# Kernel tuning notes

Measured on AMD Instinct MI355X. Metric: run time of the kernel, lower is better.

Reference implementation:

```python
import jax, jax.numpy as jnp
import numpy as np

B, G, K, N, M, E, L = 8, 512, 64, 1024, 128, 4, 5

def _lin(x, w, b):
    return x @ w.T + b

def setup_inputs():
    key = jax.random.key(0)
    ks = jax.random.split(key, 20)
    def nrm(k, shape, s=1.0):
        return jax.random.normal(k, shape, dtype=jnp.float32) * s
    def lin_p(k, out_d, in_d):
        k1, k2 = jax.random.split(k)
        s = 1.0 / float(np.sqrt(in_d))
        return nrm(k1, (out_d, in_d), s), nrm(k2, (out_d,), s)
    inp = {}
    inp["z"] = nrm(ks[0], (B, G, K, M), 0.5)
    inp["hs_grid"] = nrm(ks[1], (B, G, M))
    inp["hs_key"] = nrm(ks[2], (B, K, M))
    inp["lig_rep"] = nrm(ks[3], (B, E))
    inp["hs_rec"] = nrm(ks[4], (B, N, M))
    inp["w_Rl"] = jnp.ones((1,), dtype=jnp.float32)
    inp["w_mask"] = jax.random.randint(ks[5], (B, K), 0, 2)
    dims = {"wra": (M, M), "wrh": (M, M), "wla": (M, M), "wlh": (M, M),
            "z1": (1, M), "wcR": (M, M), "wcl": (M, M), "kR": (M, M),
            "mapL": (L, 2 * M + E), "fin": (1, L)}
    for i, nm in enumerate(dims):
        w, b = lin_p(ks[6 + i], *dims[nm])
        inp[nm + "_w"] = w
        inp[nm + "_b"] = b
    return inp

def reference(z, hs_grid, hs_key, lig_rep, hs_rec, w_Rl, w_mask,
              wra_w, wra_b, wrh_w, wrh_b, wla_w, wla_b, wlh_w, wlh_b,
              z1_w, z1_b, wcR_w, wcR_b, wcl_w, wcl_b, kR_w, kR_b,
              mapL_w, mapL_b, fin_w, fin_b):
    exp_z = jnp.exp(z)                                    # [B,G,K,M]
    zr = exp_z / exp_z.sum(axis=-2, keepdims=True)        # pseudo-softmax over K
    ra = jnp.einsum('bgkm,bkm->bgm', zr, hs_key)          # [B,G,M]
    zl = exp_z / exp_z.sum(axis=-3, keepdims=True)        # pseudo-softmax over G
    la = jnp.einsum('bgkm,bgm->bkm', zl, hs_grid)         # [B,K,M]
    ra_rh = _lin(ra, wra_w, wra_b) + _lin(hs_grid, wrh_w, wrh_b)  # [B,G,M]
    la_lh = _lin(la, wla_w, wla_b) + _lin(hs_key, wlh_w, wlh_b)   # [B,K,M]
    att = _lin(z, z1_w, z1_b)[..., 0]                     # [B,G,K]
    att_l = jax.nn.softmax(att, axis=2).sum(axis=1)       # [B,K]
    att_r = jax.nn.softmax(att, axis=1).sum(axis=2)       # [B,G]
    key_rep = jnp.einsum('bk,bkm->bm', att_l, la_lh)      # [B,M]
    grid_rep = jnp.einsum('bg,bgm->bm', att_r, ra_rh)     # [B,M]
    Rh = _lin(hs_rec, wcR_w, wcR_b)                       # [B,N,M]
    lh = _lin(hs_key, wcl_w, wcl_b)                       # [B,K,M]
    z_Rl = jnp.einsum('bnh,bkh->bnk', Rh, lh)             # [B,N,K]
    masked = jnp.where(w_mask[:, None, :] == 0, jnp.float32(-1e10), w_Rl * z_Rl)
    z_Rl = jax.nn.softmax(masked, axis=1)                 # softmax over N
    kfr = jnp.einsum('bnk,bnh->bkh', z_Rl, hs_rec)        # [B,K,M]
    kfr = _lin(kfr, kR_w, kR_b)
    kfr = jnp.einsum('bk,bkh->bh', att_l, kfr)            # [B,M]
    key_rep = key_rep + kfr
    pair_rep = jnp.concatenate([key_rep, lig_rep, grid_rep], axis=1)  # [B,2M+E]
    pair_rep = _lin(pair_rep, mapL_w, mapL_b)             # [B,L]
    return _lin(pair_rep, fin_w, fin_b)[..., 0]           # [B]
```

## Files before the change

### kernel.cpp

```cpp
#include <hip/hip_runtime.h>

#define Bb 8
#define Gg 512
#define Kk 64
#define Nn 1024
#define Mm 128
#define KM (Kk * Mm)
#define GPB 16
#define NCH (Gg / GPB)

struct P7 { const float* p[7]; };

__global__ __launch_bounds__(1024) void kA(
    const float* __restrict__ z, const float* __restrict__ hs_grid,
    const float* __restrict__ hs_key, const float* __restrict__ z1w,
    P7 ptrs, float* __restrict__ wT,
    float* __restrict__ raOut, float* __restrict__ attOut,
    float* __restrict__ laNum, float* __restrict__ laDen)
{
  __shared__ __align__(16) float smem[18432];
  const int bid = blockIdx.x;
  const int t = threadIdx.x;

  if (bid >= Bb * NCH) {
    float* tile = smem;
    const int r = bid - Bb * NCH;
    const int mat = r >> 4, tl = r & 15;
    const int xo = (tl & 3) * 32, y0 = (tl >> 2) * 32;
    const int tx = t & 31, ty = t >> 5;
    const float* src = ptrs.p[mat];
    float* dst = wT + (size_t)mat * Mm * Mm;
    tile[ty * 33 + tx] = src[(size_t)(y0 + ty) * Mm + xo + tx];
    __syncthreads();
    dst[(size_t)(xo + ty) * Mm + y0 + tx] = tile[tx * 33 + ty];
    return;
  }

  float* s_hskey  = smem;
  float* s_hsgrid = smem + 8192;
  float* s_rn     = smem + 10240;
  float* s_rd     = smem + 14336;

  const int b = bid >> 5;
  const int gblk = bid & 31;
  const int lane_m = t & 31;
  const int m4 = lane_m << 2;
  const int kgrp = t >> 5;
  const int wv = t >> 6;

  const float* hkb = hs_key + (size_t)b * KM;
  for (int idx = t; idx < KM; idx += 1024) s_hskey[idx] = hkb[idx];
  const float* hgb = hs_grid + ((size_t)b * Gg + gblk * GPB) * Mm;
  for (int idx = t; idx < GPB * Mm; idx += 1024) s_hsgrid[idx] = hgb[idx];

  const float zw0 = z1w[m4], zw1 = z1w[m4 + 1], zw2 = z1w[m4 + 2], zw3 = z1w[m4 + 3];

  float la_n[2][4], la_d[2][4];
#pragma unroll
  for (int i = 0; i < 2; ++i)
#pragma unroll
    for (int j = 0; j < 4; ++j) { la_n[i][j] = 0.f; la_d[i][j] = 0.f; }

  const float* zb = z + ((size_t)b * Gg + gblk * GPB) * (size_t)Mm * Kk;
  const int ofs0 = (kgrp * 2) * Mm + m4;
  const int ofs1 = ofs0 + Mm;
  float4 c0 = *reinterpret_cast<const float4*>(zb + ofs0);
  float4 c1 = *reinterpret_cast<const float4*>(zb + ofs1);

  __syncthreads();

  for (int gl = 0; gl < GPB; ++gl) {
    float4 n0 = c0, n1 = c1;
    if (gl < GPB - 1) {
      n0 = *reinterpret_cast<const float4*>(zb + (size_t)(gl + 1) * KM + ofs0);
      n1 = *reinterpret_cast<const float4*>(zb + (size_t)(gl + 1) * KM + ofs1);
    }
    const int g = gblk * GPB + gl;
    const float4 hg = *reinterpret_cast<const float4*>(s_hsgrid + gl * Mm + m4);
    float rn0 = 0, rn1 = 0, rn2 = 0, rn3 = 0, rd0 = 0, rd1 = 0, rd2 = 0, rd3 = 0;
#pragma unroll
    for (int i = 0; i < 2; ++i) {
      const float4 v = (i == 0) ? c0 : c1;
      const int k = kgrp * 2 + i;
      const float e0 = __expf(v.x), e1 = __expf(v.y), e2 = __expf(v.z), e3 = __expf(v.w);
      la_n[i][0] += e0 * hg.x; la_n[i][1] += e1 * hg.y; la_n[i][2] += e2 * hg.z; la_n[i][3] += e3 * hg.w;
      la_d[i][0] += e0;        la_d[i][1] += e1;        la_d[i][2] += e2;        la_d[i][3] += e3;
      const float4 hk = *reinterpret_cast<const float4*>(s_hskey + k * Mm + m4);
      rn0 += e0 * hk.x; rn1 += e1 * hk.y; rn2 += e2 * hk.z; rn3 += e3 * hk.w;
      rd0 += e0; rd1 += e1; rd2 += e2; rd3 += e3;
      float ap = v.x * zw0 + v.y * zw1 + v.z * zw2 + v.w * zw3;
      ap += __shfl_xor(ap, 16); ap += __shfl_xor(ap, 8); ap += __shfl_xor(ap, 4);
      ap += __shfl_xor(ap, 2);  ap += __shfl_xor(ap, 1);
      if (lane_m == 0) attOut[((size_t)b * Gg + g) * Kk + k] = ap;
    }
    rn0 += __shfl_xor(rn0, 32); rn1 += __shfl_xor(rn1, 32); rn2 += __shfl_xor(rn2, 32); rn3 += __shfl_xor(rn3, 32);
    rd0 += __shfl_xor(rd0, 32); rd1 += __shfl_xor(rd1, 32); rd2 += __shfl_xor(rd2, 32); rd3 += __shfl_xor(rd3, 32);
    float* rnB = s_rn + (gl & 1) * 2048;
    float* rdB = s_rd + (gl & 1) * 2048;
    if ((t & 63) < 32) {
      *reinterpret_cast<float4*>(rnB + wv * Mm + m4) = make_float4(rn0, rn1, rn2, rn3);
      *reinterpret_cast<float4*>(rdB + wv * Mm + m4) = make_float4(rd0, rd1, rd2, rd3);
    }
    __syncthreads();
    if (t < Mm) {
      float num = 0.f, den = 0.f;
#pragma unroll
      for (int ww = 0; ww < 16; ++ww) { num += rnB[ww * Mm + t]; den += rdB[ww * Mm + t]; }
      raOut[((size_t)b * Gg + g) * Mm + t] = num / den;
    }
    c0 = n0; c1 = n1;
  }

  const size_t base = ((size_t)(b * NCH + gblk)) * KM;
#pragma unroll
  for (int i = 0; i < 2; ++i) {
    const int k = kgrp * 2 + i;
    *reinterpret_cast<float4*>(laNum + base + k * Mm + m4) =
        make_float4(la_n[i][0], la_n[i][1], la_n[i][2], la_n[i][3]);
    *reinterpret_cast<float4*>(laDen + base + k * Mm + m4) =
        make_float4(la_d[i][0], la_d[i][1], la_d[i][2], la_d[i][3]);
  }
}

__global__ __launch_bounds__(256) void kB(
    const float* __restrict__ laNum, const float* __restrict__ laDen, float* __restrict__ la,
    const float* __restrict__ att, float* __restrict__ attlP,
    float* __restrict__ attrPM, float* __restrict__ attrPS,
    const float* __restrict__ hs_key, const float* __restrict__ wT,
    const float* __restrict__ wcR_w, const float* __restrict__ wcl_b,
    float* __restrict__ Lk)
{
  __shared__ __align__(16) float smem[1088];
  const int bid = blockIdx.x;
  const int t = threadIdx.x;

  if (bid < 256) {
    const int idx = bid * 256 + t;
    const int b = idx >> 13, r = idx & 8191;
    const float* np = laNum + (size_t)b * NCH * KM + r;
    const float* dp = laDen + (size_t)b * NCH * KM + r;
    float num = 0.f, den = 0.f;
#pragma unroll 8
    for (int p = 0; p < NCH; ++p) { num += np[(size_t)p * KM]; den += dp[(size_t)p * KM]; }
    la[idx] = num / den;
  } else if (bid < 320) {
    const int blk = bid - 256;
    const int b = blk >> 3, p = blk & 7;
    const int w = t >> 6, lane = t & 63;
    float acc = 0.f;
    for (int j = 0; j < 16; ++j) {
      const int g = p * 64 + w * 16 + j;
      const float a = att[((size_t)b * Gg + g) * Kk + lane];
      float mx = a;
      for (int off = 32; off; off >>= 1) mx = fmaxf(mx, __shfl_xor(mx, off));
      const float e = __expf(a - mx);
      float s = e;
      for (int off = 32; off; off >>= 1) s += __shfl_xor(s, off);
      acc += e / s;
    }
    float* sred = smem;
    sred[w * 64 + lane] = acc;
    __syncthreads();
    if (t < 64) attlP[(b * 8 + p) * 64 + t] = sred[t] + sred[64 + t] + sred[128 + t] + sred[192 + t];
  } else if (bid < 384) {
    const int blk = bid - 320;
    const int b = blk >> 3, gc = blk & 7;
    const int k = t & 63, j4 = t >> 6;
    float m = -1e30f, s = 0.f;
    for (int j = 0; j < 16; ++j) {
      const int g = gc * 64 + j4 * 16 + j;
      const float a = att[((size_t)b * Gg + g) * Kk + k];
      if (a > m) { s = s * __expf(m - a) + 1.0f; m = a; }
      else s += __expf(a - m);
    }
    float* sm = smem;
    float* ss = smem + 256;
    sm[j4 * 64 + k] = m; ss[j4 * 64 + k] = s;
    __syncthreads();
    if (t < 64) {
      float M = sm[t];
      for (int q = 1; q < 4; ++q) M = fmaxf(M, sm[q * 64 + t]);
      float S = 0.f;
      for (int q = 0; q < 4; ++q) S += ss[q * 64 + t] * __expf(sm[q * 64 + t] - M);
      attrPM[(b * 8 + gc) * 64 + t] = M;
      attrPS[(b * 8 + gc) * 64 + t] = S;
    }
  } else {
    const int blk = bid - 384;
    const int b = blk >> 3, k8 = blk & 7;
    float* s_lh = smem;
    const int m = t & 127;
    const int half = __builtin_amdgcn_readfirstlane(t >> 7);
    const float* wclT = wT + 5 * 16384;
    {
      const float* keyb = hs_key + ((size_t)b * Kk + k8 * 8 + half * 4) * Mm;
      float a0 = 0.f, a1 = 0.f, a2 = 0.f, a3 = 0.f;
      for (int h = 0; h < 128; ++h) {
        const float w = wclT[(size_t)h * Mm + m];
        const float r0v = keyb[h];
        const float r1v = keyb[128 + h];
        const float r2v = keyb[256 + h];
        const float r3v = keyb[384 + h];
        a0 += r0v * w; a1 += r1v * w; a2 += r2v * w; a3 += r3v * w;
      }
      const float bm = wcl_b[m];
      s_lh[(half * 4 + 0) * 132 + m] = a0 + bm;
      s_lh[(half * 4 + 1) * 132 + m] = a1 + bm;
      s_lh[(half * 4 + 2) * 132 + m] = a2 + bm;
      s_lh[(half * 4 + 3) * 132 + m] = a3 + bm;
    }
    __syncthreads();
    {
      const int h = m;
      const int r0 = half * 4;
      float b0 = 0.f, b1 = 0.f, b2 = 0.f, b3 = 0.f;
      for (int mq = 0; mq < 32; ++mq) {
        const float4 L0 = *reinterpret_cast<const float4*>(&s_lh[(r0 + 0) * 132 + mq * 4]);
        const float4 L1 = *reinterpret_cast<const float4*>(&s_lh[(r0 + 1) * 132 + mq * 4]);
        const float4 L2 = *reinterpret_cast<const float4*>(&s_lh[(r0 + 2) * 132 + mq * 4]);
        const float4 L3 = *reinterpret_cast<const float4*>(&s_lh[(r0 + 3) * 132 + mq * 4]);
        const float w0 = wcR_w[(size_t)(mq * 4 + 0) * Mm + h];
        const float w1 = wcR_w[(size_t)(mq * 4 + 1) * Mm + h];
        const float w2 = wcR_w[(size_t)(mq * 4 + 2) * Mm + h];
        const float w3 = wcR_w[(size_t)(mq * 4 + 3) * Mm + h];
        b0 += L0.x * w0 + L0.y * w1 + L0.z * w2 + L0.w * w3;
        b1 += L1.x * w0 + L1.y * w1 + L1.z * w2 + L1.w * w3;
        b2 += L2.x * w0 + L2.y * w1 + L2.z * w2 + L2.w * w3;
        b3 += L3.x * w0 + L3.y * w1 + L3.z * w2 + L3.w * w3;
      }
      const size_t ob = ((size_t)b * Kk + k8 * 8 + r0) * Mm + h;
      Lk[ob] = b0; Lk[ob + Mm] = b1; Lk[ob + 2 * Mm] = b2; Lk[ob + 3 * Mm] = b3;
    }
  }
}

__global__ __launch_bounds__(256) void kC(
    const float* __restrict__ att, const float* __restrict__ attrPM, const float* __restrict__ attrPS,
    float* __restrict__ att_r,
    const float* __restrict__ hs_rec, const float* __restrict__ Lk,
    const int* __restrict__ mask, const float* __restrict__ wRl,
    float* __restrict__ scores, float* __restrict__ pmT, float* __restrict__ psT)
{
  __shared__ __align__(16) float smem[4608];
  const int bid = blockIdx.x;
  const int t = threadIdx.x;

  if (bid < 64) {
    const int b = bid >> 3, gc = bid & 7;
    const int k = t & 63, grp = t >> 6;
    float* Mx = smem;
    float* S = smem + 64;
    if (t < 64) {
      float M = -1e30f;
      for (int p = 0; p < 8; ++p) M = fmaxf(M, attrPM[(b * 8 + p) * 64 + t]);
      float s = 0.f;
      for (int p = 0; p < 8; ++p) s += attrPS[(b * 8 + p) * 64 + t] * __expf(attrPM[(b * 8 + p) * 64 + t] - M);
      Mx[t] = M; S[t] = s;
    }
    __syncthreads();
    const float Mk = Mx[k], Sk = S[k];
    for (int j = 0; j < 16; ++j) {
      const int g = gc * 64 + grp * 16 + j;
      float p = __expf(att[((size_t)b * Gg + g) * Kk + k] - Mk) / Sk;
      for (int off = 32; off; off >>= 1) p += __shfl_xor(p, off);
      if (k == 0) att_r[b * Gg + g] = p;
    }
  } else {
    const int vb = bid - 64;
    const int b = vb >> 6, ntile = vb & 63;
    const int n0 = ntile * 16;
    const int k = t & 63;
    const int hq = __builtin_amdgcn_readfirstlane(t >> 6);
    float rLk[32];
    {
      const float* Lp = Lk + ((size_t)b * Kk + k) * Mm + hq * 32;
#pragma unroll
      for (int j = 0; j < 8; ++j) {
        const float4 v = *reinterpret_cast<const float4*>(Lp + j * 4);
        rLk[j * 4 + 0] = v.x; rLk[j * 4 + 1] = v.y;
        rLk[j * 4 + 2] = v.z; rLk[j * 4 + 3] = v.w;
      }
    }
    float acc[16];
    const float* rb = hs_rec + ((size_t)b * Nn + n0) * Mm + hq * 32;
#pragma unroll
    for (int r = 0; r < 16; ++r) {
      const float* rp = rb + r * Mm;
      float s = 0.f;
#pragma unroll
      for (int j = 0; j < 32; ++j) s += rp[j] * rLk[j];
      acc[r] = s;
    }
    float* s_acc = smem;
    float* s_m   = smem + 4096;
    float* s_s   = smem + 4352;
#pragma unroll
    for (int r = 0; r < 16; ++r) s_acc[(hq * 16 + r) * 64 + k] = acc[r];
    __syncthreads();
    const float wv = wRl[0];
    const bool msk = (mask[b * Kk + k] == 0);
    float m = -3.0e38f, ssum = 0.f;
    for (int q = 0; q < 4; ++q) {
      const int idx = q * 256 + t;
      const int r = idx >> 6, kk = idx & 63;
      float v = s_acc[r * 64 + kk] + s_acc[(16 + r) * 64 + kk] +
                s_acc[(32 + r) * 64 + kk] + s_acc[(48 + r) * 64 + kk];
      v = msk ? -1e10f : wv * v;
      scores[((size_t)b * Nn + n0 + r) * Kk + kk] = v;
      if (v > m) { ssum = ssum * __expf(m - v) + 1.0f; m = v; }
      else ssum += __expf(v - m);
    }
    s_m[hq * 64 + k] = m; s_s[hq * 64 + k] = ssum;
    __syncthreads();
    if (t < 64) {
      float M = fmaxf(fmaxf(s_m[t], s_m[64 + t]), fmaxf(s_m[128 + t], s_m[192 + t]));
      float S = 0.f;
#pragma unroll
      for (int q = 0; q < 4; ++q) S += s_s[q * 64 + t] * __expf(s_m[q * 64 + t] - M);
      pmT[((size_t)b * 64 + ntile) * 64 + t] = M;
      psT[((size_t)b * 64 + ntile) * 64 + t] = S;
    }
  }
}

__global__ __launch_bounds__(512) void kD(
    const float* __restrict__ scores, const float* __restrict__ hs_rec,
    const float* __restrict__ pmT, const float* __restrict__ psT,
    const float* __restrict__ attlP, const float* __restrict__ att_r,
    const float* __restrict__ ra, const float* __restrict__ hs_grid,
    const float* __restrict__ la, const float* __restrict__ hs_key,
    float* __restrict__ uP, float* __restrict__ w1P, float* __restrict__ w2P,
    float* __restrict__ w0P, float* __restrict__ v1, float* __restrict__ v2,
    float* __restrict__ sAv)
{
  __shared__ float sm[1280];
  __shared__ float s_attl[64];
  __shared__ float sM[64], sSi[64];
  const int bid = blockIdx.x;
  const int t = threadIdx.x;

  if (bid < 64) {
    const int b = bid >> 3, nc = bid & 7;
    if (t < 64) {
      float a = 0.f;
      for (int p = 0; p < 8; ++p) a += attlP[(b * 8 + p) * 64 + t];
      s_attl[t] = a;
      float M = -3.0e38f;
      for (int nt = 0; nt < 64; ++nt) M = fmaxf(M, pmT[((size_t)b * 64 + nt) * 64 + t]);
      float S = 0.f;
      for (int nt = 0; nt < 64; ++nt)
        S += psT[((size_t)b * 64 + nt) * 64 + t] * __expf(pmT[((size_t)b * 64 + nt) * 64 + t] - M);
      sM[t] = M; sSi[t] = 1.0f / S;
    }
    __syncthreads();
    const int n = t >> 2, ks = t & 3;
    const float* sc = scores + ((size_t)b * Nn + nc * 128 + n) * Kk + ks * 16;
    float qp = 0.f;
#pragma unroll
    for (int j = 0; j < 16; ++j) {
      const int k = ks * 16 + j;
      qp += s_attl[k] * __expf(sc[j] - sM[k]) * sSi[k];
    }
    sm[n * 4 + ks] = qp;
    __syncthreads();
    float* q = sm + 512;
    if (t < 128) q[t] = sm[t * 4] + sm[t * 4 + 1] + sm[t * 4 + 2] + sm[t * 4 + 3];
    __syncthreads();
    const int h = t & 127, nq = t >> 7;
    float acc = 0.f;
    const float* hr = hs_rec + ((size_t)b * Nn + nc * 128 + nq * 32) * Mm + h;
    for (int j = 0; j < 32; ++j) acc += q[nq * 32 + j] * hr[(size_t)j * Mm];
    float* red = sm + 640;
    red[nq * 128 + h] = acc;
    __syncthreads();
    if (t < 128) uP[((size_t)b * 8 + nc) * 128 + t] = red[t] + red[128 + t] + red[256 + t] + red[384 + t];
  } else if (bid < 128) {
    const int blk = bid - 64;
    const int b = blk >> 3, gc = blk & 7;
    float* s_ar = sm + 1152;
    if (t < 64) s_ar[t] = att_r[b * Gg + gc * 64 + t];
    __syncthreads();
    const int h = t & 127, gq = t >> 7;
    float a1 = 0.f, a2 = 0.f;
    const float* rp = ra + ((size_t)b * Gg + gc * 64 + gq * 16) * Mm + h;
    const float* gp = hs_grid + ((size_t)b * Gg + gc * 64 + gq * 16) * Mm + h;
    for (int j = 0; j < 16; ++j) {
      const float w = s_ar[gq * 16 + j];
      a1 += w * rp[(size_t)j * Mm];
      a2 += w * gp[(size_t)j * Mm];
    }
    float* r1 = sm;
    float* r2 = sm + 512;
    r1[gq * 128 + h] = a1; r2[gq * 128 + h] = a2;
    __syncthreads();
    if (t < 128) {
      w1P[((size_t)b * 8 + gc) * 128 + t] = r1[t] + r1[128 + t] + r1[256 + t] + r1[384 + t];
      w2P[((size_t)b * 8 + gc) * 128 + t] = r2[t] + r2[128 + t] + r2[256 + t] + r2[384 + t];
    }
    if (t == 0) {
      float s = 0.f;
      for (int j = 0; j < 64; ++j) s += s_ar[j];
      w0P[b * 8 + gc] = s;
    }
  } else {
    const int b = bid - 128;
    if (t < 64) {
      float a = 0.f;
      for (int p = 0; p < 8; ++p) a += attlP[(b * 8 + p) * 64 + t];
      s_attl[t] = a;
    }
    __syncthreads();
    const int h = t & 127, kq = t >> 7;
    float a1 = 0.f, a2 = 0.f;
    const float* lp = la + ((size_t)b * Kk + kq * 16) * Mm + h;
    const float* kp = hs_key + ((size_t)b * Kk + kq * 16) * Mm + h;
    for (int j = 0; j < 16; ++j) {
      const float w = s_attl[kq * 16 + j];
      a1 += w * lp[(size_t)j * Mm];
      a2 += w * kp[(size_t)j * Mm];
    }
    float* r1 = sm;
    float* r2 = sm + 512;
    r1[kq * 128 + h] = a1; r2[kq * 128 + h] = a2;
    __syncthreads();
    if (t < 128) {
      v1[b * 128 + t] = r1[t] + r1[128 + t] + r1[256 + t] + r1[384 + t];
      v2[b * 128 + t] = r2[t] + r2[128 + t] + r2[256 + t] + r2[384 + t];
    }
    if (t == 0) {
      float s = 0.f;
      for (int j = 0; j < 64; ++j) s += s_attl[j];
      sAv[b] = s;
    }
  }
}

__global__ __launch_bounds__(256) void kE(
    const float* __restrict__ uP, const float* __restrict__ w1P, const float* __restrict__ w2P,
    const float* __restrict__ w0P, const float* __restrict__ v1, const float* __restrict__ v2,
    const float* __restrict__ sAv, const float* __restrict__ wT,
    const float* __restrict__ wra_b, const float* __restrict__ wrh_b,
    const float* __restrict__ wla_b, const float* __restrict__ wlh_b,
    const float* __restrict__ kR_b, const float* __restrict__ lig_rep,
    const float* __restrict__ mapL_w, const float* __restrict__ mapL_b,
    const float* __restrict__ fin_w, const float* __restrict__ fin_b,
    float* __restrict__ out)
{
  __shared__ float sV1[128], sV2[128], sU[128], sW1[128], sW2[128];
  __shared__ float sPair[260];
  __shared__ float sRed[2][2][128];
  __shared__ float s5[8];
  __shared__ float sSc[2];
  const int b = blockIdx.x, t = threadIdx.x;
  const int m = t & 127, hf = t >> 7;

  if (t < 128) {
    float u = 0.f, w1 = 0.f, w2 = 0.f;
    for (int c = 0; c < 8; ++c) {
      u  += uP[((size_t)b * 8 + c) * 128 + t];
      w1 += w1P[((size_t)b * 8 + c) * 128 + t];
      w2 += w2P[((size_t)b * 8 + c) * 128 + t];
    }
    sU[t] = u; sW1[t] = w1; sW2[t] = w2;
    sV1[t] = v1[b * 128 + t]; sV2[t] = v2[b * 128 + t];
  }
  if (t == 0) {
    float s = 0.f;
    for (int c = 0; c < 8; ++c) s += w0P[b * 8 + c];
    sSc[0] = s;
    sSc[1] = sAv[b];
  }
  __syncthreads();

  const float* wraT = wT;
  const float* wrhT = wT + 1 * 16384;
  const float* wlaT = wT + 2 * 16384;
  const float* wlhT = wT + 3 * 16384;
  const float* kRT  = wT + 6 * 16384;
  float key = 0.f, grd = 0.f;
  for (int h = hf * 64; h < hf * 64 + 64; ++h) {
    key += sV1[h] * wlaT[h * Mm + m] + sV2[h] * wlhT[h * Mm + m] + sU[h] * kRT[h * Mm + m];
    grd += sW1[h] * wraT[h * Mm + m] + sW2[h] * wrhT[h * Mm + m];
  }
  sRed[0][hf][m] = key; sRed[1][hf][m] = grd;
  __syncthreads();
  if (t < 128) {
    const float sR = sSc[0], sA = sSc[1];
    sPair[t] = sRed[0][0][t] + sRed[0][1][t] + sA * (wla_b[t] + wlh_b[t] + kR_b[t]);
    sPair[132 + t] = sRed[1][0][t] + sRed[1][1][t] + sR * (wra_b[t] + wrh_b[t]);
  }
  if (t < 4) sPair[128 + t] = lig_rep[b * 4 + t];
  __syncthreads();

  const int wv = t >> 6, lane = t & 63;
  for (int l = wv; l < 5; l += 4) {
    float acc = 0.f;
    for (int c = lane; c < 260; c += 64) acc += sPair[c] * mapL_w[l * 260 + c];
    for (int off = 32; off; off >>= 1) acc += __shfl_xor(acc, off);
    if (lane == 0) s5[l] = acc + mapL_b[l];
  }
  __syncthreads();
  if (t == 0) {
    float o = fin_b[0];
    for (int l = 0; l < 5; ++l) o += s5[l] * fin_w[l];
    out[b] = o;
  }
}

extern "C" void kernel_launch(void* const* d_in, const int* in_sizes, int n_in,
                              void* d_out, int out_size, void* d_ws, size_t ws_size,
                              hipStream_t stream) {
  const float* z       = (const float*)d_in[0];
  const float* hs_grid = (const float*)d_in[1];
  const float* hs_key  = (const float*)d_in[2];
  const float* lig_rep = (const float*)d_in[3];
  const float* hs_rec  = (const float*)d_in[4];
  const float* w_Rl    = (const float*)d_in[5];
  const int*   w_mask  = (const int*)d_in[6];
  const float* wra_w = (const float*)d_in[7];  const float* wra_b = (const float*)d_in[8];
  const float* wrh_w = (const float*)d_in[9];  const float* wrh_b = (const float*)d_in[10];
  const float* wla_w = (const float*)d_in[11]; const float* wla_b = (const float*)d_in[12];
  const float* wlh_w = (const float*)d_in[13]; const float* wlh_b = (const float*)d_in[14];
  const float* z1_w  = (const float*)d_in[15];
  const float* wcR_w = (const float*)d_in[17]; const float* wcR_b = (const float*)d_in[18];
  const float* wcl_w = (const float*)d_in[19]; const float* wcl_b = (const float*)d_in[20];
  const float* kR_w  = (const float*)d_in[21]; const float* kR_b  = (const float*)d_in[22];
  const float* mapL_w = (const float*)d_in[23]; const float* mapL_b = (const float*)d_in[24];
  const float* fin_w  = (const float*)d_in[25]; const float* fin_b  = (const float*)d_in[26];
  float* out = (float*)d_out;

  float* w = (float*)d_ws;
  float* wT    = w;
  float* ra    = wT + 7 * 16384;
  float* att   = ra + Bb * Gg * Mm;
  float* laNum = att + Bb * Gg * Kk;
  float* laDen = laNum + Bb * NCH * Kk * Mm;
  float* la    = laDen + Bb * NCH * Kk * Mm;
  float* attlP = la + Bb * Kk * Mm;
  float* attrPM = attlP + Bb * 8 * 64;
  float* attrPS = attrPM + Bb * 8 * 64;
  float* att_r = attrPS + Bb * 8 * 64;
  float* Lk    = att_r + Bb * Gg;
  float* scores = Lk + Bb * Kk * Mm;

  float* pmT  = laNum;
  float* psT  = laNum + 32768;
  float* uP   = laNum + 65536;
  float* w1P  = laNum + 73728;
  float* w2P  = laNum + 81920;
  float* w0P  = laNum + 90112;
  float* v1   = laNum + 90176;
  float* v2   = laNum + 91200;
  float* sAv  = laNum + 92224;

  P7 ptrs;
  ptrs.p[0] = wra_w; ptrs.p[1] = wrh_w; ptrs.p[2] = wla_w; ptrs.p[3] = wlh_w;
  ptrs.p[4] = wcR_w; ptrs.p[5] = wcl_w; ptrs.p[6] = kR_w;

  kA<<<Bb * NCH + 112, 1024, 0, stream>>>(z, hs_grid, hs_key, z1_w, ptrs, wT,
                                          ra, att, laNum, laDen);
  kB<<<448, 256, 0, stream>>>(laNum, laDen, la, att, attlP, attrPM, attrPS,
                              hs_key, wT, wcR_w, wcl_b, Lk);
  kC<<<576, 256, 0, stream>>>(att, attrPM, attrPS, att_r, hs_rec, Lk,
                              w_mask, w_Rl, scores, pmT, psT);
  kD<<<136, 512, 0, stream>>>(scores, hs_rec, pmT, psT, attlP, att_r,
                              ra, hs_grid, la, hs_key,
                              uP, w1P, w2P, w0P, v1, v2, sAv);
  kE<<<Bb, 256, 0, stream>>>(uP, w1P, w2P, w0P, v1, v2, sAv, wT,
                             wra_b, wrh_b, wla_b, wlh_b, kR_b, lig_rep,
                             mapL_w, mapL_b, fin_w, fin_b, out);
}
```

Baseline: 91.59 us.

## Fuse five kernels into one cooperative kernel with grid-wide syncs

Merges the five separate stage kernels into a single cooperative launch of 256 blocks of 1024 threads, using grid.sync between stages. Later stages pack several former small blocks into each large block as 256- or 512-thread virtual blocks, each with its own shared-memory slice. The weight transpose now runs after the main z pass on the same blocks rather than on extra blocks. This removes per-launch overhead and inter-kernel gaps, at the cost of grid-barrier latency and leaving many blocks idle in the lighter stages.

```diff
diff --git a/kernel.cpp b/kernel.cpp
--- a/kernel.cpp
+++ b/kernel.cpp
@@ -1,572 +1,548 @@
 #include <hip/hip_runtime.h>
+#include <hip/hip_cooperative_groups.h>
+
+namespace cg = cooperative_groups;
 
 #define Bb 8
 #define Gg 512
 #define Kk 64
 #define Nn 1024
 #define Mm 128
-#define KM (Kk * Mm)
+#define KM 8192
 #define GPB 16
-#define NCH (Gg / GPB)
-
-struct P7 { const float* p[7]; };
-
-__global__ __launch_bounds__(1024) void kA(
-    const float* __restrict__ z, const float* __restrict__ hs_grid,
-    const float* __restrict__ hs_key, const float* __restrict__ z1w,
-    P7 ptrs, float* __restrict__ wT,
-    float* __restrict__ raOut, float* __restrict__ attOut,
-    float* __restrict__ laNum, float* __restrict__ laDen)
-{
+#define NCH 32
+
+struct Args {
+  const float *z, *hs_grid, *hs_key, *z1w;
+  const float *wsrc[7];
+  const float *wcR_w, *wcl_b;
+  const float *hs_rec;
+  const int   *mask;
+  const float *wRl;
+  const float *wra_b, *wrh_b, *wla_b, *wlh_b, *kR_b, *lig_rep;
+  const float *mapL_w, *mapL_b, *fin_w, *fin_b;
+  float *wT, *ra, *att, *laNum, *laDen, *la;
+  float *attlP, *attrPM, *attrPS, *att_r, *Lk, *scores;
+  float *pmT, *psT, *uP, *w1P, *w2P, *w0P, *v1, *v2, *sAv;
+  float *out;
+};
+
+__global__ __launch_bounds__(1024) void fused(Args a) {
+  cg::grid_group grid = cg::this_grid();
   __shared__ __align__(16) float smem[18432];
   const int bid = blockIdx.x;
   const int t = threadIdx.x;
 
-  if (bid >= Bb * NCH) {
+  {
+    float* s_hskey  = smem;
+    float* s_hsgrid = smem + 8192;
+    float* s_rn     = smem + 10240;
+    float* s_rd     = smem + 14336;
+
+    const int b = bid >> 5;
+    const int gblk = bid & 31;
+    const int lane_m = t & 31;
+    const int m4 = lane_m << 2;
+    const int kgrp = t >> 5;
+    const int wv = t >> 6;
+
+    const float* hkb = a.hs_key + (size_t)b * KM;
+    for (int idx = t; idx < KM; idx += 1024) s_hskey[idx] = hkb[idx];
+    const float* hgb = a.hs_grid + ((size_t)b * Gg + gblk * GPB) * Mm;
+    for (int idx = t; idx < GPB * Mm; idx += 1024) s_hsgrid[idx] = hgb[idx];
+
+    const float zw0 = a.z1w[m4], zw1 = a.z1w[m4 + 1], zw2 = a.z1w[m4 + 2], zw3 = a.z1w[m4 + 3];
+
+    float la_n[2][4], la_d[2][4];
+#pragma unroll
+    for (int i = 0; i < 2; ++i)
+#pragma unroll
+      for (int j = 0; j < 4; ++j) { la_n[i][j] = 0.f; la_d[i][j] = 0.f; }
+
+    const float* zb = a.z + ((size_t)b * Gg + gblk * GPB) * (size_t)KM;
+    const int ofs0 = (kgrp * 2) * Mm + m4;
+    const int ofs1 = ofs0 + Mm;
+    float4 c0 = *reinterpret_cast<const float4*>(zb + ofs0);
+    float4 c1 = *reinterpret_cast<const float4*>(zb + ofs1);
+
+    __syncthreads();
+
+    for (int gl = 0; gl < GPB; ++gl) {
+      float4 n0 = c0, n1 = c1;
+      if (gl < GPB - 1) {
+        n0 = *reinterpret_cast<const float4*>(zb + (size_t)(gl + 1) * KM + ofs0);
+        n1 = *reinterpret_cast<const float4*>(zb + (size_t)(gl + 1) * KM + ofs1);
+      }
+      const int g = gblk * GPB + gl;
+      const float4 hg = *reinterpret_cast<const float4*>(s_hsgrid + gl * Mm + m4);
+      float rn0 = 0, rn1 = 0, rn2 = 0, rn3 = 0, rd0 = 0, rd1 = 0, rd2 = 0, rd3 = 0;
+#pragma unroll
+      for (int i = 0; i < 2; ++i) {
+        const float4 v = (i == 0) ? c0 : c1;
+        const int k = kgrp * 2 + i;
+        const float e0 = __expf(v.x), e1 = __expf(v.y), e2 = __expf(v.z), e3 = __expf(v.w);
+        la_n[i][0] += e0 * hg.x; la_n[i][1] += e1 * hg.y; la_n[i][2] += e2 * hg.z; la_n[i][3] += e3 * hg.w;
+        la_d[i][0] += e0;        la_d[i][1] += e1;        la_d[i][2] += e2;        la_d[i][3] += e3;
+        const float4 hk = *reinterpret_cast<const float4*>(s_hskey + k * Mm + m4);
+        rn0 += e0 * hk.x; rn1 += e1 * hk.y; rn2 += e2 * hk.z; rn3 += e3 * hk.w;
+        rd0 += e0; rd1 += e1; rd2 += e2; rd3 += e3;
+        float ap = v.x * zw0 + v.y * zw1 + v.z * zw2 + v.w * zw3;
+        ap += __shfl_xor(ap, 16); ap += __shfl_xor(ap, 8); ap += __shfl_xor(ap, 4);
+        ap += __shfl_xor(ap, 2);  ap += __shfl_xor(ap, 1);
+        if (lane_m == 0) a.att[((size_t)b * Gg + g) * Kk + k] = ap;
+      }
+      rn0 += __shfl_xor(rn0, 32); rn1 += __shfl_xor(rn1, 32); rn2 += __shfl_xor(rn2, 32); rn3 += __shfl_xor(rn3, 32);
+      rd0 += __shfl_xor(rd0, 32); rd1 += __shfl_xor(rd1, 32); rd2 += __shfl_xor(rd2, 32); rd3 += __shfl_xor(rd3, 32);
+      float* rnB = s_rn + (gl & 1) * 2048;
+      float* rdB = s_rd + (gl & 1) * 2048;
+      if ((t & 63) < 32) {
+        *reinterpret_cast<float4*>(rnB + wv * Mm + m4) = make_float4(rn0, rn1, rn2, rn3);
+        *reinterpret_cast<float4*>(rdB + wv * Mm + m4) = make_float4(rd0, rd1, rd2, rd3);
+      }
+      __syncthreads();
+      if (t < Mm) {
+        float num = 0.f, den = 0.f;
+#pragma unroll
+        for (int ww = 0; ww < 16; ++ww) { num += rnB[ww * Mm + t]; den += rdB[ww * Mm + t]; }
+        a.ra[((size_t)b * Gg + g) * Mm + t] = num / den;
+      }
+      c0 = n0; c1 = n1;
+    }
+
+    const size_t base = ((size_t)(b * NCH + gblk)) * KM;
+#pragma unroll
+    for (int i = 0; i < 2; ++i) {
+      const int k = kgrp * 2 + i;
+      *reinterpret_cast<float4*>(a.laNum + base + k * Mm + m4) =
+          make_float4(la_n[i][0], la_n[i][1], la_n[i][2], la_n[i][3]);
+      *reinterpret_cast<float4*>(a.laDen + base + k * Mm + m4) =
+          make_float4(la_d[i][0], la_d[i][1], la_d[i][2], la_d[i][3]);
+    }
+  }
+  __syncthreads();
+  if (bid < 112) {
     float* tile = smem;
-    const int r = bid - Bb * NCH;
-    const int mat = r >> 4, tl = r & 15;
+    const int mat = bid >> 4, tl = bid & 15;
     const int xo = (tl & 3) * 32, y0 = (tl >> 2) * 32;
     const int tx = t & 31, ty = t >> 5;
-    const float* src = ptrs.p[mat];
-    float* dst = wT + (size_t)mat * Mm * Mm;
+    const float* src = a.wsrc[mat];
+    float* dst = a.wT + (size_t)mat * Mm * Mm;
     tile[ty * 33 + tx] = src[(size_t)(y0 + ty) * Mm + xo + tx];
     __syncthreads();
     dst[(size_t)(xo + ty) * Mm + y0 + tx] = tile[tx * 33 + ty];
-    return;
   }
-
-  float* s_hskey  = smem;
-  float* s_hsgrid = smem + 8192;
-  float* s_rn     = smem + 10240;
-  float* s_rd     = smem + 14336;
-
-  const int b = bid >> 5;
-  const int gblk = bid & 31;
-  const int lane_m = t & 31;
-  const int m4 = lane_m << 2;
-  const int kgrp = t >> 5;
-  const int wv = t >> 6;
-
-  const float* hkb = hs_key + (size_t)b * KM;
-  for (int idx = t; idx < KM; idx += 1024) s_hskey[idx] = hkb[idx];
-  const float* hgb = hs_grid + ((size_t)b * Gg + gblk * GPB) * Mm;
-  for (int idx = t; idx < GPB * Mm; idx += 1024) s_hsgrid[idx] = hgb[idx];
-
-  const float zw0 = z1w[m4], zw1 = z1w[m4 + 1], zw2 = z1w[m4 + 2], zw3 = z1w[m4 + 3];
-
-  float la_n[2][4], la_d[2][4];
-#pragma unroll
-  for (int i = 0; i < 2; ++i)
-#pragma unroll
-    for (int j = 0; j < 4; ++j) { la_n[i][j] = 0.f; la_d[i][j] = 0.f; }
-
-  const float* zb = z + ((size_t)b * Gg + gblk * GPB) * (size_t)Mm * Kk;
-  const int ofs0 = (kgrp * 2) * Mm + m4;
-  const int ofs1 = ofs0 + Mm;
-  float4 c0 = *reinterpret_cast<const float4*>(zb + ofs0);
-  float4 c1 = *reinterpret_cast<const float4*>(zb + ofs1);
-
-  __syncthreads();
-
-  for (int gl = 0; gl < GPB; ++gl) {
-    float4 n0 = c0, n1 = c1;
-    if (gl < GPB - 1) {
-      n0 = *reinterpret_cast<const float4*>(zb + (size_t)(gl + 1) * KM + ofs0);
-      n1 = *reinterpret_cast<const float4*>(zb + (size_t)(gl + 1) * KM + ofs1);
-    }
-    const int g = gblk * GPB + gl;
-    const float4 hg = *reinterpret_cast<const float4*>(s_hsgrid + gl * Mm + m4);
-    float rn0 = 0, rn1 = 0, rn2 = 0, rn3 = 0, rd0 = 0, rd1 = 0, rd2 = 0, rd3 = 0;
-#pragma unroll
-    for (int i = 0; i < 2; ++i) {
-      const float4 v = (i == 0) ? c0 : c1;
-      const int k = kgrp * 2 + i;
-      const float e0 = __expf(v.x), e1 = __expf(v.y), e2 = __expf(v.z), e3 = __expf(v.w);
-      la_n[i][0] += e0 * hg.x; la_n[i][1] += e1 * hg.y; la_n[i][2] += e2 * hg.z; la_n[i][3] += e3 * hg.w;
-      la_d[i][0] += e0;        la_d[i][1] += e1;        la_d[i][2] += e2;        la_d[i][3] += e3;
-      const float4 hk = *reinterpret_cast<const float4*>(s_hskey + k * Mm + m4);
-      rn0 += e0 * hk.x; rn1 += e1 * hk.y; rn2 += e2 * hk.z; rn3 += e3 * hk.w;
-      rd0 += e0; rd1 += e1; rd2 += e2; rd3 += e3;
-      float ap = v.x * zw0 + v.y * zw1 + v.z * zw2 + v.w * zw3;
-      ap += __shfl_xor(ap, 16); ap += __shfl_xor(ap, 8); ap += __shfl_xor(ap, 4);
-      ap += __shfl_xor(ap, 2);  ap += __shfl_xor(ap, 1);
-      if (lane_m == 0) attOut[((size_t)b * Gg + g) * Kk + k] = ap;
-    }
-    rn0 += __shfl_xor(rn0, 32); rn1 += __shfl_xor(rn1, 32); rn2 += __shfl_xor(rn2, 32); rn3 += __shfl_xor(rn3, 32);
-    rd0 += __shfl_xor(rd0, 32); rd1 += __shfl_xor(rd1, 32); rd2 += __shfl_xor(rd2, 32); rd3 += __shfl_xor(rd3, 32);
-    float* rnB = s_rn + (gl & 1) * 2048;
-    float* rdB = s_rd + (gl & 1) * 2048;
-    if ((t & 63) < 32) {
-      *reinterpret_cast<float4*>(rnB + wv * Mm + m4) = make_float4(rn0, rn1, rn2, rn3);
-      *reinterpret_cast<float4*>(rdB + wv * Mm + m4) = make_float4(rd0, rd1, rd2, rd3);
+  grid.sync();
+
+  if (bid < 112) {
+    const int vb = (bid << 2) | (t >> 8);
+    const int vt = t & 255;
+    float* smp = smem + (t >> 8) * 1088;
+    if (vb < 256) {
+      const int idx = vb * 256 + vt;
+      const int b = idx >> 13, r = idx & 8191;
+      const float* np = a.laNum + (size_t)b * NCH * KM + r;
+      const float* dp = a.laDen + (size_t)b * NCH * KM + r;
+      float num = 0.f, den = 0.f;
+#pragma unroll 8
+      for (int p = 0; p < NCH; ++p) { num += np[(size_t)p * KM]; den += dp[(size_t)p * KM]; }
+      a.la[idx] = num / den;
+    } else if (vb < 320) {
+      const int blk = vb - 256;
+      const int b = blk >> 3, p = blk & 7;
+      const int w = vt >> 6, lane = vt & 63;
+      float acc = 0.f;
+      for (int j = 0; j < 16; ++j) {
+        const int g = p * 64 + w * 16 + j;
+        const float av = a.att[((size_t)b * Gg + g) * Kk + lane];
+        float mx = av;
+        for (int off = 32; off; off >>= 1) mx = fmaxf(mx, __shfl_xor(mx, off));
+        const float e = __expf(av - mx);
+        float s = e;
+        for (int off = 32; off; off >>= 1) s += __shfl_xor(s, off);
+        acc += e / s;
+      }
+      smp[w * 64 + lane] = acc;
+      __syncthreads();
+      if (vt < 64) a.attlP[(b * 8 + p) * 64 + vt] = smp[vt] + smp[64 + vt] + smp[128 + vt] + smp[192 + vt];
+    } else if (vb < 384) {
+      const int blk = vb - 320;
+      const int b = blk >> 3, gc = blk & 7;
+      const int k = vt & 63, j4 = vt >> 6;
+      float m = -1e30f, s = 0.f;
+      for (int j = 0; j < 16; ++j) {
+        const int g = gc * 64 + j4 * 16 + j;
+        const float av = a.att[((size_t)b * Gg + g) * Kk + k];
+        if (av > m) { s = s * __expf(m - av) + 1.0f; m = av; }
+        else s += __expf(av - m);
+      }
+      float* sm = smp;
+      float* ss = smp + 256;
+      sm[j4 * 64 + k] = m; ss[j4 * 64 + k] = s;
+      __syncthreads();
+      if (vt < 64) {
+        float M = sm[vt];
+        for (int q = 1; q < 4; ++q) M = fmaxf(M, sm[q * 64 + vt]);
+        float S = 0.f;
+        for (int q = 0; q < 4; ++q) S += ss[q * 64 + vt] * __expf(sm[q * 64 + vt] - M);
+        a.attrPM[(b * 8 + gc) * 64 + vt] = M;
+        a.attrPS[(b * 8 + gc) * 64 + vt] = S;
+      }
+    } else {
+      const int blk = vb - 384;
+      const int b = blk >> 3, k8 = blk & 7;
+      float* s_lh = smp;
+      const int m = vt & 127;
+      const int half = __builtin_amdgcn_readfirstlane(vt >> 7);
+      const float* wclT = a.wT + 5 * 16384;
+      {
+        const float* keyb = a.hs_key + ((size_t)b * Kk + k8 * 8 + half * 4) * Mm;
+        float a0 = 0.f, a1 = 0.f, a2 = 0.f, a3 = 0.f;
+        for (int h = 0; h < 128; ++h) {
+          const float w = wclT[(size_t)h * Mm + m];
+          const float r0v = keyb[h];
+          const float r1v = keyb[128 + h];
+          const float r2v = keyb[256 + h];
+          const float r3v = keyb[384 + h];
+          a0 += r0v * w; a1 += r1v * w; a2 += r2v * w; a3 += r3v * w;
+        }
+        const float bm = a.wcl_b[m];
+        s_lh[(half * 4 + 0) * 132 + m] = a0 + bm;
+        s_lh[(half * 4 + 1) * 132 + m] = a1 + bm;
+        s_lh[(half * 4 + 2) * 132 + m] = a2 + bm;
+        s_lh[(half * 4 + 3) * 132 + m] = a3 + bm;
+      }
+      __syncthreads();
+      {
+        const int h = m;
+        const int r0 = half * 4;
+        float b0 = 0.f, b1 = 0.f, b2 = 0.f, b3 = 0.f;
+        for (int mq = 0; mq < 32; ++mq) {
+          const float4 L0 = *reinterpret_cast<const float4*>(&s_lh[(r0 + 0) * 132 + mq * 4]);
+          const float4 L1 = *reinterpret_cast<const float4*>(&s_lh[(r0 + 1) * 132 + mq * 4]);
+          const float4 L2 = *reinterpret_cast<const float4*>(&s_lh[(r0 + 2) * 132 + mq * 4]);
+          const float4 L3 = *reinterpret_cast<const float4*>(&s_lh[(r0 + 3) * 132 + mq * 4]);
+          const float w0 = a.wcR_w[(size_t)(mq * 4 + 0) * Mm + h];
+          const float w1 = a.wcR_w[(size_t)(mq * 4 + 1) * Mm + h];
+          const float w2 = a.wcR_w[(size_t)(mq * 4 + 2) * Mm + h];
+          const float w3 = a.wcR_w[(size_t)(mq * 4 + 3) * Mm + h];
+          b0 += L0.x * w0 + L0.y * w1 + L0.z * w2 + L0.w * w3;
+          b1 += L1.x * w0 + L1.y * w1 + L1.z * w2 + L1.w * w3;
+          b2 += L2.x * w0 + L2.y * w1 + L2.z * w2 + L2.w * w3;
+          b3 += L3.x * w0 + L3.y * w1 + L3.z * w2 + L3.w * w3;
+        }
+        const size_t ob = ((size_t)b * Kk + k8 * 8 + r0) * Mm + h;
+        a.Lk[ob] = b0; a.Lk[ob + Mm] = b1; a.Lk[ob + 2 * Mm] = b2; a.Lk[ob + 3 * Mm] = b3;
+      }
+    }
+  }
+  grid.sync();
+
+  if (bid < 144) {
+    const int vb = (bid << 2) | (t >> 8);
+    const int vt = t & 255;
+    float* smp = smem + (t >> 8) * 4608;
+    if (vb < 64) {
+      const int b = vb >> 3, gc = vb & 7;
+      const int k = vt & 63, grp = vt >> 6;
+      float* Mx = smp;
+      float* S = smp + 64;
+      if (vt < 64) {
+        float M = -1e30f;
+        for (int p = 0; p < 8; ++p) M = fmaxf(M, a.attrPM[(b * 8 + p) * 64 + vt]);
+        float s = 0.f;
+        for (int p = 0; p < 8; ++p) s += a.attrPS[(b * 8 + p) * 64 + vt] * __expf(a.attrPM[(b * 8 + p) * 64 + vt] - M);
+        Mx[vt] = M; S[vt] = s;
+      }
+      __syncthreads();
+      const float Mk = Mx[k], Sk = S[k];
+      for (int j = 0; j < 16; ++j) {
+        const int g = gc * 64 + grp * 16 + j;
+        float p = __expf(a.att[((size_t)b * Gg + g) * Kk + k] - Mk) / Sk;
+        for (int off = 32; off; off >>= 1) p += __shfl_xor(p, off);
+        if (k == 0) a.att_r[b * Gg + g] = p;
+      }
+      __syncthreads();
+    } else {
+      const int vbs = vb - 64;
+      const int b = vbs >> 6, ntile = vbs & 63;
+      const int n0 = ntile * 16;
+      const int k = vt & 63;
+      const int hq = __builtin_amdgcn_readfirstlane(vt >> 6);
+      float rLk[32];
+      {
+        const float* Lp = a.Lk + ((size_t)b * Kk + k) * Mm + hq * 32;
+#pragma unroll
+        for (int j = 0; j < 8; ++j) {
+          const float4 v = *reinterpret_cast<const float4*>(Lp + j * 4);
+          rLk[j * 4 + 0] = v.x; rLk[j * 4 + 1] = v.y;
+          rLk[j * 4 + 2] = v.z; rLk[j * 4 + 3] = v.w;
+        }
+      }
+      float acc[16];
+      const float* rb = a.hs_rec + ((size_t)b * Nn + n0) * Mm + hq * 32;
+#pragma unroll
+      for (int r = 0; r < 16; ++r) {
+        const float* rp = rb + r * Mm;
+        float s = 0.f;
+#pragma unroll
+        for (int j = 0; j < 32; ++j) s += rp[j] * rLk[j];
+        acc[r] = s;
+      }
+      float* s_acc = smp;
+      float* s_m   = smp + 4096;
+      float* s_s   = smp + 4352;
+#pragma unroll
+      for (int r = 0; r < 16; ++r) s_acc[(hq * 16 + r) * 64 + k] = acc[r];
+      __syncthreads();
+      const float wv = a.wRl[0];
+      const bool msk = (a.mask[b * Kk + k] == 0);
+      float m = -3.0e38f, ssum = 0.f;
+      for (int q = 0; q < 4; ++q) {
+        const int idx = q * 256 + vt;
+        const int r = idx >> 6, kk = idx & 63;
+        float v = s_acc[r * 64 + kk] + s_acc[(16 + r) * 64 + kk] +
+                  s_acc[(32 + r) * 64 + kk] + s_acc[(48 + r) * 64 + kk];
+        v = msk ? -1e10f : wv * v;
+        a.scores[((size_t)b * Nn + n0 + r) * Kk + kk] = v;
+        if (v > m) { ssum = ssum * __expf(m - v) + 1.0f; m = v; }
+        else ssum += __expf(v - m);
+      }
+      s_m[hq * 64 + k] = m; s_s[hq * 64 + k] = ssum;
+      __syncthreads();
+      if (vt < 64) {
+        float M = fmaxf(fmaxf(s_m[vt], s_m[64 + vt]), fmaxf(s_m[128 + vt], s_m[192 + vt]));
+        float S = 0.f;
+#pragma unroll
+        for (int q = 0; q < 4; ++q) S += s_s[q * 64 + vt] * __expf(s_m[q * 64 + vt] - M);
+        a.pmT[((size_t)b * 64 + ntile) * 64 + vt] = M;
+        a.psT[((size_t)b * 64 + ntile) * 64 + vt] = S;
+      }
+    }
+  }
+  grid.sync();
+
+  if (bid < 68) {
+    const int vb = (bid << 1) | (t >> 9);
+    const int vt = t & 511;
+    float* smp = smem + (t >> 9) * 1472;
+    float* sm = smp;
+    float* s_attl = smp + 1280;
+    float* sM = smp + 1344;
+    float* sSi = smp + 1408;
+    if (vb < 64) {
+      const int b = vb >> 3, nc = vb & 7;
+      if (vt < 64) {
+        float aa = 0.f;
+        for (int p = 0; p < 8; ++p) aa += a.attlP[(b * 8 + p) * 64 + vt];
+        s_attl[vt] = aa;
+        float M = -3.0e38f;
+        for (int nt = 0; nt < 64; ++nt) M = fmaxf(M, a.pmT[((size_t)b * 64 + nt) * 64 + vt]);
+        float S = 0.f;
+        for (int nt = 0; nt < 64; ++nt)
+          S += a.psT[((size_t)b * 64 + nt) * 64 + vt] * __expf(a.pmT[((size_t)b * 64 + nt) * 64 + vt] - M);
+        sM[vt] = M; sSi[vt] = 1.0f / S;
+      }
+      __syncthreads();
+      const int n = vt >> 2, ks = vt & 3;
+      const float* sc = a.scores + ((size_t)b * Nn + nc * 128 + n) * Kk + ks * 16;
+      float qp = 0.f;
+#pragma unroll
+      for (int j = 0; j < 16; ++j) {
+        const int k = ks * 16 + j;
+        qp += s_attl[k] * __expf(sc[j] - sM[k]) * sSi[k];
+      }
+      sm[n * 4 + ks] = qp;
+      __syncthreads();
+      float* q = sm + 512;
+      if (vt < 128) q[vt] = sm[vt * 4] + sm[vt * 4 + 1] + sm[vt * 4 + 2] + sm[vt * 4 + 3];
+      __syncthreads();
+      const int h = vt & 127, nq = vt >> 7;
+      float acc = 0.f;
+      const float* hr = a.hs_rec + ((size_t)b * Nn + nc * 128 + nq * 32) * Mm + h;
+      for (int j = 0; j < 32; ++j) acc += q[nq * 32 + j] * hr[(size_t)j * Mm];
+      float* red = sm + 640;
+      red[nq * 128 + h] = acc;
+      __syncthreads();
+      if (vt < 128) a.uP[((size_t)b * 8 + nc) * 128 + vt] = red[vt] + red[128 + vt] + red[256 + vt] + red[384 + vt];
+    } else if (vb < 128) {
+      const int blk = vb - 64;
+      const int b = blk >> 3, gc = blk & 7;
+      float* s_ar = sm + 1152;
+      if (vt < 64) s_ar[vt] = a.att_r[b * Gg + gc * 64 + vt];
+      __syncthreads();
+      const int h = vt & 127, gq = vt >> 7;
+      float a1 = 0.f, a2 = 0.f;
+      const float* rp = a.ra + ((size_t)b * Gg + gc * 64 + gq * 16) * Mm + h;
+      const float* gp = a.hs_grid + ((size_t)b * Gg + gc * 64 + gq * 16) * Mm + h;
+      for (int j = 0; j < 16; ++j) {
+        const float w = s_ar[gq * 16 + j];
+        a1 += w * rp[(size_t)j * Mm];
+        a2 += w * gp[(size_t)j * Mm];
+      }
+      float* r1 = sm;
+      float* r2 = sm + 512;
+      r1[gq * 128 + h] = a1; r2[gq * 128 + h] = a2;
+      __syncthreads();
+      if (vt < 128) {
+        a.w1P[((size_t)b * 8 + gc) * 128 + vt] = r1[vt] + r1[128 + vt] + r1[256 + vt] + r1[384 + vt];
+        a.w2P[((size_t)b * 8 + gc) * 128 + vt] = r2[vt] + r2[128 + vt] + r2[256 + vt] + r2[384 + vt];
+      }
+      if (vt == 0) {
+        float s = 0.f;
+        for (int j = 0; j < 64; ++j) s += s_ar[j];
+        a.w0P[b * 8 + gc] = s;
+      }
+    } else {
+      const int b = vb - 128;
+      if (vt < 64) {
+        float aa = 0.f;
+        for (int p = 0; p < 8; ++p) aa += a.attlP[(b * 8 + p) * 64 + vt];
+        s_attl[vt] = aa;
+      }
+      __syncthreads();
+      const int h = vt & 127, kq = vt >> 7;
+      float a1 = 0.f, a2 = 0.f;
+      const float* lp = a.la + ((size_t)b * Kk + kq * 16) * Mm + h;
+      const float* kp = a.hs_key + ((size_t)b * Kk + kq * 16) * Mm + h;
+      for (int j = 0; j < 16; ++j) {
+        const float w = s_attl[kq * 16 + j];
+        a1 += w * lp[(size_t)j * Mm];
+        a2 += w * kp[(size_t)j * Mm];
+      }
+      float* r1 = sm;
+      float* r2 = sm + 512;
+      r1[kq * 128 + h] = a1; r2[kq * 128 + h] = a2;
+      __syncthreads();
+      if (vt < 128) {
+        a.v1[b * 128 + vt] = r1[vt] + r1[128 + vt] + r1[256 + vt] + r1[384 + vt];
+        a.v2[b * 128 + vt] = r2[vt] + r2[128 + vt] + r2[256 + vt] + r2[384 + vt];
+      }
+      if (vt == 0) {
+        float s = 0.f;
+        for (int j = 0; j < 64; ++j) s += s_attl[j];
+        a.sAv[b] = s;
+      }
+    }
+  }
+  grid.sync();
+
+  if (bid < 2) {
+    const int vb = (bid << 2) | (t >> 8);
+    const int vt = t & 255;
+    float* smp = smem + (t >> 8) * 1440;
+    float* sV1 = smp;          float* sV2 = smp + 128;
+    float* sU  = smp + 256;    float* sW1 = smp + 384;  float* sW2 = smp + 512;
+    float* sPair = smp + 640;
+    float* sRed  = smp + 904;
+    float* s5    = smp + 1416;
+    float* sSc   = smp + 1424;
+    const int b = vb;
+    const int m = vt & 127, hf = vt >> 7;
+
+    if (vt < 128) {
+      float u = 0.f, w1 = 0.f, w2 = 0.f;
+      for (int c = 0; c < 8; ++c) {
+        u  += a.uP[((size_t)b * 8 + c) * 128 + vt];
+        w1 += a.w1P[((size_t)b * 8 + c) * 128 + vt];
+        w2 += a.w2P[((size_t)b * 8 + c) * 128 + vt];
+      }
+      sU[vt] = u; sW1[vt] = w1; sW2[vt] = w2;
+      sV1[vt] = a.v1[b * 128 + vt]; sV2[vt] = a.v2[b * 128 + vt];
+    }
+    if (vt == 0) {
+      float s = 0.f;
+      for (int c = 0; c < 8; ++c) s += a.w0P[b * 8 + c];
+      sSc[0] = s;
+      sSc[1] = a.sAv[b];
     }
     __syncthreads();
-    if (t < Mm) {
-      float num = 0.f, den = 0.f;
-#pragma unroll
-      for (int ww = 0; ww < 16; ++ww) { num += rnB[ww * Mm + t]; den += rdB[ww * Mm + t]; }
-      raOut[((size_t)b * Gg + g) * Mm + t] = num / den;
-    }
-    c0 = n0; c1 = n1;
-  }
-
-  const size_t base = ((size_t)(b * NCH + gblk)) * KM;
-#pragma unroll
-  for (int i = 0; i < 2; ++i) {
-    const int k = kgrp * 2 + i;
-    *reinterpret_cast<float4*>(laNum + base + k * Mm + m4) =
-        make_float4(la_n[i][0], la_n[i][1], la_n[i][2], la_n[i][3]);
-    *reinterpret_cast<float4*>(laDen + base + k * Mm + m4) =
-        make_float4(la_d[i][0], la_d[i][1], la_d[i][2], la_d[i][3]);
-  }
-}
-
-__global__ __launch_bounds__(256) void kB(
-    const float* __restrict__ laNum, const float* __restrict__ laDen, float* __restrict__ la,
-    const float* __restrict__ att, float* __restrict__ attlP,
-    float* __restrict__ attrPM, float* __restrict__ attrPS,
-    const float* __restrict__ hs_key, const float* __restrict__ wT,
-    const float* __restrict__ wcR_w, const float* __restrict__ wcl_b,
-    float* __restrict__ Lk)
-{
-  __shared__ __align__(16) float smem[1088];
-  const int bid = blockIdx.x;
-  const int t = threadIdx.x;
-
-  if (bid < 256) {
-    const int idx = bid * 256 + t;
-    const int b = idx >> 13, r = idx & 8191;
-    const float* np = laNum + (size_t)b * NCH * KM + r;
-    const float* dp = laDen + (size_t)b * NCH * KM + r;
-    float num = 0.f, den = 0.f;
-#pragma unroll 8
-    for (int p = 0; p < NCH; ++p) { num += np[(size_t)p * KM]; den += dp[(size_t)p * KM]; }
-    la[idx] = num / den;
-  } else if (bid < 320) {
-    const int blk = bid - 256;
-    const int b = blk >> 3, p = blk & 7;
-    const int w = t >> 6, lane = t & 63;
-    float acc = 0.f;
-    for (int j = 0; j < 16; ++j) {
-      const int g = p * 64 + w * 16 + j;
-      const float a = att[((size_t)b * Gg + g) * Kk + lane];
-      float mx = a;
-      for (int off = 32; off; off >>= 1) mx = fmaxf(mx, __shfl_xor(mx, off));
-      const float e = __expf(a - mx);
-      float s = e;
-      for (int off = 32; off; off >>= 1) s += __shfl_xor(s, off);
-      acc += e / s;
-    }
-    float* sred = smem;
-    sred[w * 64 + lane] = acc;
+
+    const float* wraT = a.wT;
+    const float* wrhT = a.wT + 1 * 16384;
+    const float* wlaT = a.wT + 2 * 16384;
+    const float* wlhT = a.wT + 3 * 16384;
+    const float* kRT  = a.wT + 6 * 16384;
+    float key = 0.f, grd = 0.f;
+    for (int h = hf * 64; h < hf * 64 + 64; ++h) {
+      key += sV1[h] * wlaT[h * Mm + m] + sV2[h] * wlhT[h * Mm + m] + sU[h] * kRT[h * Mm + m];
+      grd += sW1[h] * wraT[h * Mm + m] + sW2[h] * wrhT[h * Mm + m];
+    }
+    sRed[0 * 256 + hf * 128 + m] = key;
+    sRed[1 * 256 + hf * 128 + m] = grd;
     __syncthreads();
-    if (t < 64) attlP[(b * 8 + p) * 64 + t] = sred[t] + sred[64 + t] + sred[128 + t] + sred[192 + t];
-  } else if (bid < 384) {
-    const int blk = bid - 320;
-    const int b = blk >> 3, gc = blk & 7;
-    const int k = t & 63, j4 = t >> 6;
-    float m = -1e30f, s = 0.f;
-    for (int j = 0; j < 16; ++j) {
-      const int g = gc * 64 + j4 * 16 + j;
-      const float a = att[((size_t)b * Gg + g) * Kk + k];
-      if (a > m) { s = s * __expf(m - a) + 1.0f; m = a; }
-      else s += __expf(a - m);
-    }
-    float* sm = smem;
-    float* ss = smem + 256;
-    sm[j4 * 64 + k] = m; ss[j4 * 64 + k] = s;
+    if (vt < 128) {
+      const float sR = sSc[0], sA = sSc[1];
+      sPair[vt] = sRed[vt] + sRed[128 + vt] + sA * (a.wla_b[vt] + a.wlh_b[vt] + a.kR_b[vt]);
+      sPair[132 + vt] = sRed[256 + vt] + sRed[384 + vt] + sR * (a.wra_b[vt] + a.wrh_b[vt]);
+    }
+    if (vt < 4) sPair[128 + vt] = a.lig_rep[b * 4 + vt];
     __syncthreads();
-    if (t < 64) {
-      float M = sm[t];
-      for (int q = 1; q < 4; ++q) M = fmaxf(M, sm[q * 64 + t]);
-      float S = 0.f;
-      for (int q = 0; q < 4; ++q) S += ss[q * 64 + t] * __expf(sm[q * 64 + t] - M);
-      attrPM[(b * 8 + gc) * 64 + t] = M;
-      attrPS[(b * 8 + gc) * 64 + t] = S;
-    }
-  } else {
-    const int blk = bid - 384;
-    const int b = blk >> 3, k8 = blk & 7;
-    float* s_lh = smem;
-    const int m = t & 127;
-    const int half = __builtin_amdgcn_readfirstlane(t >> 7);
-    const float* wclT = wT + 5 * 16384;
-    {
-      const float* keyb = hs_key + ((size_t)b * Kk + k8 * 8 + half * 4) * Mm;
-      float a0 = 0.f, a1 = 0.f, a2 = 0.f, a3 = 0.f;
-      for (int h = 0; h < 128; ++h) {
-        const float w = wclT[(size_t)h * Mm + m];
-        const float r0v = keyb[h];
-        const float r1v = keyb[128 + h];
-        const float r2v = keyb[256 + h];
-        const float r3v = keyb[384 + h];
-        a0 += r0v * w; a1 += r1v * w; a2 += r2v * w; a3 += r3v * w;
-      }
-      const float bm = wcl_b[m];
-      s_lh[(half * 4 + 0) * 132 + m] = a0 + bm;
-      s_lh[(half * 4 + 1) * 132 + m] = a1 + bm;
-      s_lh[(half * 4 + 2) * 132 + m] = a2 + bm;
-      s_lh[(half * 4 + 3) * 132 + m] = a3 + bm;
+
+    const int wq = vt >> 6, lane = vt & 63;
+    for (int l = wq; l < 5; l += 4) {
+      float acc = 0.f;
+      for (int c = lane; c < 260; c += 64) acc += sPair[c] * a.mapL_w[l * 260 + c];
+      for (int off = 32; off; off >>= 1) acc += __shfl_xor(acc, off);
+      if (lane == 0) s5[l] = acc + a.mapL_b[l];
     }
     __syncthreads();
-    {
-      const int h = m;
-      const int r0 = half * 4;
-      float b0 = 0.f, b1 = 0.f, b2 = 0.f, b3 = 0.f;
-      for (int mq = 0; mq < 32; ++mq) {
-        const float4 L0 = *reinterpret_cast<const float4*>(&s_lh[(r0 + 0) * 132 + mq * 4]);
-        const float4 L1 = *reinterpret_cast<const float4*>(&s_lh[(r0 + 1) * 132 + mq * 4]);
-        const float4 L2 = *reinterpret_cast<const float4*>(&s_lh[(r0 + 2) * 132 + mq * 4]);
-        const float4 L3 = *reinterpret_cast<const float4*>(&s_lh[(r0 + 3) * 132 + mq * 4]);
-        const float w0 = wcR_w[(size_t)(mq * 4 + 0) * Mm + h];
-        const float w1 = wcR_w[(size_t)(mq * 4 + 1) * Mm + h];
-        const float w2 = wcR_w[(size_t)(mq * 4 + 2) * Mm + h];
-        const float w3 = wcR_w[(size_t)(mq * 4 + 3) * Mm + h];
-        b0 += L0.x * w0 + L0.y * w1 + L0.z * w2 + L0.w * w3;
-        b1 += L1.x * w0 + L1.y * w1 + L1.z * w2 + L1.w * w3;
-        b2 += L2.x * w0 + L2.y * w1 + L2.z * w2 + L2.w * w3;
-        b3 += L3.x * w0 + L3.y * w1 + L3.z * w2 + L3.w * w3;
-      }
-      const size_t ob = ((size_t)b * Kk + k8 * 8 + r0) * Mm + h;
-      Lk[ob] = b0; Lk[ob + Mm] = b1; Lk[ob + 2 * Mm] = b2; Lk[ob + 3 * Mm] = b3;
-    }
-  }
-}
-
-__global__ __launch_bounds__(256) void kC(
-    const float* __restrict__ att, const float* __restrict__ attrPM, const float* __restrict__ attrPS,
-    float* __restrict__ att_r,
-    const float* __restrict__ hs_rec, const float* __restrict__ Lk,
-    const int* __restrict__ mask, const float* __restrict__ wRl,
-    float* __restrict__ scores, float* __restrict__ pmT, float* __restrict__ psT)
-{
-  __shared__ __align__(16) float smem[4608];
-  const int bid = blockIdx.x;
-  const int t = threadIdx.x;
-
-  if (bid < 64) {
-    const int b = bid >> 3, gc = bid & 7;
-    const int k = t & 63, grp = t >> 6;
-    float* Mx = smem;
-    float* S = smem + 64;
-    if (t < 64) {
-      float M = -1e30f;
-      for (int p = 0; p < 8; ++p) M = fmaxf(M, attrPM[(b * 8 + p) * 64 + t]);
-      float s = 0.f;
-      for (int p = 0; p < 8; ++p) s += attrPS[(b * 8 + p) * 64 + t] * __expf(attrPM[(b * 8 + p) * 64 + t] - M);
-      Mx[t] = M; S[t] = s;
-    }
-    __syncthreads();
-    const float Mk = Mx[k], Sk = S[k];
-    for (int j = 0; j < 16; ++j) {
-      const int g = gc * 64 + grp * 16 + j;
-      float p = __expf(att[((size_t)b * Gg + g) * Kk + k] - Mk) / Sk;
-      for (int off = 32; off; off >>= 1) p += __shfl_xor(p, off);
-      if (k == 0) att_r[b * Gg + g] = p;
-    }
-  } else {
-    const int vb = bid - 64;
-    const int b = vb >> 6, ntile = vb & 63;
-    const int n0 = ntile * 16;
-    const int k = t & 63;
-    const int hq = __builtin_amdgcn_readfirstlane(t >> 6);
-    float rLk[32];
-    {
-      const float* Lp = Lk + ((size_t)b * Kk + k) * Mm + hq * 32;
-#pragma unroll
-      for (int j = 0; j < 8; ++j) {
-        const float4 v = *reinterpret_cast<const float4*>(Lp + j * 4);
-        rLk[j * 4 + 0] = v.x; rLk[j * 4 + 1] = v.y;
-        rLk[j * 4 + 2] = v.z; rLk[j * 4 + 3] = v.w;
-      }
-    }
-    float acc[16];
-    const float* rb = hs_rec + ((size_t)b * Nn + n0) * Mm + hq * 32;
-#pragma unroll
-    for (int r = 0; r < 16; ++r) {
-      const float* rp = rb + r * Mm;
-      float s = 0.f;
-#pragma unroll
-      for (int j = 0; j < 32; ++j) s += rp[j] * rLk[j];
-      acc[r] = s;
-    }
-    float* s_acc = smem;
-    float* s_m   = smem + 4096;
-    float* s_s   = smem + 4352;
-#pragma unroll
-    for (int r = 0; r < 16; ++r) s_acc[(hq * 16 + r) * 64 + k] = acc[r];
-    __syncthreads();
-    const float wv = wRl[0];
-    const bool msk = (mask[b * Kk + k] == 0);
-    float m = -3.0e38f, ssum = 0.f;
-    for (int q = 0; q < 4; ++q) {
-      const int idx = q * 256 + t;
-      const int r = idx >> 6, kk = idx & 63;
-      float v = s_acc[r * 64 + kk] + s_acc[(16 + r) * 64 + kk] +
-                s_acc[(32 + r) * 64 + kk] + s_acc[(48 + r) * 64 + kk];
-      v = msk ? -1e10f : wv * v;
-      scores[((size_t)b * Nn + n0 + r) * Kk + kk] = v;
-      if (v > m) { ssum = ssum * __expf(m - v) + 1.0f; m = v; }
-      else ssum += __expf(v - m);
-    }
-    s_m[hq * 64 + k] = m; s_s[hq * 64 + k] = ssum;
-    __syncthreads();
-    if (t < 64) {
-      float M = fmaxf(fmaxf(s_m[t], s_m[64 + t]), fmaxf(s_m[128 + t], s_m[192 + t]));
-      float S = 0.f;
-#pragma unroll
-      for (int q = 0; q < 4; ++q) S += s_s[q * 64 + t] * __expf(s_m[q * 64 + t] - M);
-      pmT[((size_t)b * 64 + ntile) * 64 + t] = M;
-      psT[((size_t)b * 64 + ntile) * 64 + t] = S;
-    }
-  }
-}
-
-__global__ __launch_bounds__(512) void kD(
-    const float* __restrict__ scores, const float* __restrict__ hs_rec,
-    const float* __restrict__ pmT, const float* __restrict__ psT,
-    const float* __restrict__ attlP, const float* __restrict__ att_r,
-    const float* __restrict__ ra, const float* __restrict__ hs_grid,
-    const float* __restrict__ la, const float* __restrict__ hs_key,
-    float* __restrict__ uP, float* __restrict__ w1P, float* __restrict__ w2P,
-    float* __restrict__ w0P, float* __restrict__ v1, float* __restrict__ v2,
-    float* __restrict__ sAv)
-{
-  __shared__ float sm[1280];
-  __shared__ float s_attl[64];
-  __shared__ float sM[64], sSi[64];
-  const int bid = blockIdx.x;
-  const int t = threadIdx.x;
-
-  if (bid < 64) {
-    const int b = bid >> 3, nc = bid & 7;
-    if (t < 64) {
-      float a = 0.f;
-      for (int p = 0; p < 8; ++p) a += attlP[(b * 8 + p) * 64 + t];
-      s_attl[t] = a;
-      float M = -3.0e38f;
-      for (int nt = 0; nt < 64; ++nt) M = fmaxf(M, pmT[((size_t)b * 64 + nt) * 64 + t]);
-      float S = 0.f;
-      for (int nt = 0; nt < 64; ++nt)
-        S += psT[((size_t)b * 64 + nt) * 64 + t] * __expf(pmT[((size_t)b * 64 + nt) * 64 + t] - M);
-      sM[t] = M; sSi[t] = 1.0f / S;
-    }
-    __syncthreads();
-    const int n = t >> 2, ks = t & 3;
-    const float* sc = scores + ((size_t)b * Nn + nc * 128 + n) * Kk + ks * 16;
-    float qp = 0.f;
-#pragma unroll
-    for (int j = 0; j < 16; ++j) {
-      const int k = ks * 16 + j;
-      qp += s_attl[k] * __expf(sc[j] - sM[k]) * sSi[k];
-    }
-    sm[n * 4 + ks] = qp;
-    __syncthreads();
-    float* q = sm + 512;
-    if (t < 128) q[t] = sm[t * 4] + sm[t * 4 + 1] + sm[t * 4 + 2] + sm[t * 4 + 3];
-    __syncthreads();
-    const int h = t & 127, nq = t >> 7;
-    float acc = 0.f;
-    const float* hr = hs_rec + ((size_t)b * Nn + nc * 128 + nq * 32) * Mm + h;
-    for (int j = 0; j < 32; ++j) acc += q[nq * 32 + j] * hr[(size_t)j * Mm];
-    float* red = sm + 640;
-    red[nq * 128 + h] = acc;
-    __syncthreads();
-    if (t < 128) uP[((size_t)b * 8 + nc) * 128 + t] = red[t] + red[128 + t] + red[256 + t] + red[384 + t];
-  } else if (bid < 128) {
-    const int blk = bid - 64;
-    const int b = blk >> 3, gc = blk & 7;
-    float* s_ar = sm + 1152;
-    if (t < 64) s_ar[t] = att_r[b * Gg + gc * 64 + t];
-    __syncthreads();
-    const int h = t & 127, gq = t >> 7;
-    float a1 = 0.f, a2 = 0.f;
-    const float* rp = ra + ((size_t)b * Gg + gc * 64 + gq * 16) * Mm + h;
-    const float* gp = hs_grid + ((size_t)b * Gg + gc * 64 + gq * 16) * Mm + h;
-    for (int j = 0; j < 16; ++j) {
-      const float w = s_ar[gq * 16 + j];
-      a1 += w * rp[(size_t)j * Mm];
-      a2 += w * gp[(size_t)j * Mm];
-    }
-    float* r1 = sm;
-    float* r2 = sm + 512;
-    r1[gq * 128 + h] = a1; r2[gq * 128 + h] = a2;
-    __syncthreads();
-    if (t < 128) {
-      w1P[((size_t)b * 8 + gc) * 128 + t] = r1[t] + r1[128 + t] + r1[256 + t] + r1[384 + t];
-      w2P[((size_t)b * 8 + gc) * 128 + t] = r2[t] + r2[128 + t] + r2[256 + t] + r2[384 + t];
-    }
-    if (t == 0) {
-      float s = 0.f;
-      for (int j = 0; j < 64; ++j) s += s_ar[j];
-      w0P[b * 8 + gc] = s;
-    }
-  } else {
-    const int b = bid - 128;
-    if (t < 64) {
-      float a = 0.f;
-      for (int p = 0; p < 8; ++p) a += attlP[(b * 8 + p) * 64 + t];
-      s_attl[t] = a;
-    }
-    __syncthreads();
-    const int h = t & 127, kq = t >> 7;
-    float a1 = 0.f, a2 = 0.f;
-    const float* lp = la + ((size_t)b * Kk + kq * 16) * Mm + h;
-    const float* kp = hs_key + ((size_t)b * Kk + kq * 16) * Mm + h;
-    for (int j = 0; j < 16; ++j) {
-      const float w = s_attl[kq * 16 + j];
-      a1 += w * lp[(size_t)j * Mm];
-      a2 += w * kp[(size_t)j * Mm];
-    }
-    float* r1 = sm;
-    float* r2 = sm + 512;
-    r1[kq * 128 + h] = a1; r2[kq * 128 + h] = a2;
-    __syncthreads();
-    if (t < 128) {
-      v1[b * 128 + t] = r1[t] + r1[128 + t] + r1[256 + t] + r1[384 + t];
-      v2[b * 128 + t] = r2[t] + r2[128 + t] + r2[256 + t] + r2[384 + t];
-    }
-    if (t == 0) {
-      float s = 0.f;
-      for (int j = 0; j < 64; ++j) s += s_attl[j];
-      sAv[b] = s;
-    }
-  }
-}
-
-__global__ __launch_bounds__(256) void kE(
-    const float* __restrict__ uP, const float* __restrict__ w1P, const float* __restrict__ w2P,
-    const float* __restrict__ w0P, const float* __restrict__ v1, const float* __restrict__ v2,
-    const float* __restrict__ sAv, const float* __restrict__ wT,
-    const float* __restrict__ wra_b, const float* __restrict__ wrh_b,
-    const float* __restrict__ wla_b, const float* __restrict__ wlh_b,
-    const float* __restrict__ kR_b, const float* __restrict__ lig_rep,
-    const float* __restrict__ mapL_w, const float* __restrict__ mapL_b,
-    const float* __restrict__ fin_w, const float* __restrict__ fin_b,
-    float* __restrict__ out)
-{
-  __shared__ float sV1[128], sV2[128], sU[128], sW1[128], sW2[128];
-  __shared__ float sPair[260];
-  __shared__ float sRed[2][2][128];
-  __shared__ float s5[8];
-  __shared__ float sSc[2];
-  const int b = blockIdx.x, t = threadIdx.x;
-  const int m = t & 127, hf = t >> 7;
-
-  if (t < 128) {
-    float u = 0.f, w1 = 0.f, w2 = 0.f;
-    for (int c = 0; c < 8; ++c) {
-      u  += uP[((size_t)b * 8 + c) * 128 + t];
-      w1 += w1P[((size_t)b * 8 + c) * 128 + t];
-      w2 += w2P[((size_t)b * 8 + c) * 128 + t];
-    }
-    sU[t] = u; sW1[t] = w1; sW2[t] = w2;
-    sV1[t] = v1[b * 128 + t]; sV2[t] = v2[b * 128 + t];
-  }
-  if (t == 0) {
-    float s = 0.f;
-    for (int c = 0; c < 8; ++c) s += w0P[b * 8 + c];
-    sSc[0] = s;
-    sSc[1] = sAv[b];
-  }
-  __syncthreads();
-
-  const float* wraT = wT;
-  const float* wrhT = wT + 1 * 16384;
-  const float* wlaT = wT + 2 * 16384;
-  const float* wlhT = wT + 3 * 16384;
-  const float* kRT  = wT + 6 * 16384;
-  float key = 0.f, grd = 0.f;
-  for (int h = hf * 64; h < hf * 64 + 64; ++h) {
-    key += sV1[h] * wlaT[h * Mm + m] + sV2[h] * wlhT[h * Mm + m] + sU[h] * kRT[h * Mm + m];
-    grd += sW1[h] * wraT[h * Mm + m] + sW2[h] * wrhT[h * Mm + m];
-  }
-  sRed[0][hf][m] = key; sRed[1][hf][m] = grd;
-  __syncthreads();
-  if (t < 128) {
-    const float sR = sSc[0], sA = sSc[1];
-    sPair[t] = sRed[0][0][t] + sRed[0][1][t] + sA * (wla_b[t] + wlh_b[t] + kR_b[t]);
-    sPair[132 + t] = sRed[1][0][t] + sRed[1][1][t] + sR * (wra_b[t] + wrh_b[t]);
-  }
-  if (t < 4) sPair[128 + t] = lig_rep[b * 4 + t];
-  __syncthreads();
-
-  const int wv = t >> 6, lane = t & 63;
-  for (int l = wv; l < 5; l += 4) {
-    float acc = 0.f;
-    for (int c = lane; c < 260; c += 64) acc += sPair[c] * mapL_w[l * 260 + c];
-    for (int off = 32; off; off >>= 1) acc += __shfl_xor(acc, off);
-    if (lane == 0) s5[l] = acc + mapL_b[l];
-  }
-  __syncthreads();
-  if (t == 0) {
-    float o = fin_b[0];
-    for (int l = 0; l < 5; ++l) o += s5[l] * fin_w[l];
-    out[b] = o;
+    if (vt == 0) {
+      float o = a.fin_b[0];
+      for (int l = 0; l < 5; ++l) o += s5[l] * a.fin_w[l];
+      a.out[b] = o;
+    }
   }
 }
 
 extern "C" void kernel_launch(void* const* d_in, const int* in_sizes, int n_in,
                               void* d_out, int out_size, void* d_ws, size_t ws_size,
                               hipStream_t stream) {
-  const float* z       = (const float*)d_in[0];
-  const float* hs_grid = (const float*)d_in[1];
-  const float* hs_key  = (const float*)d_in[2];
-  const float* lig_rep = (const float*)d_in[3];
-  const float* hs_rec  = (const float*)d_in[4];
-  const float* w_Rl    = (const float*)d_in[5];
-  const int*   w_mask  = (const int*)d_in[6];
-  const float* wra_w = (const float*)d_in[7];  const float* wra_b = (const float*)d_in[8];
-  const float* wrh_w = (const float*)d_in[9];  const float* wrh_b = (const float*)d_in[10];
-  const float* wla_w = (const float*)d_in[11]; const float* wla_b = (const float*)d_in[12];
-  const float* wlh_w = (const float*)d_in[13]; const float* wlh_b = (const float*)d_in[14];
-  const float* z1_w  = (const float*)d_in[15];
-  const float* wcR_w = (const float*)d_in[17]; const float* wcR_b = (const float*)d_in[18];
-  const float* wcl_w = (const float*)d_in[19]; const float* wcl_b = (const float*)d_in[20];
-  const float* kR_w  = (const float*)d_in[21]; const float* kR_b  = (const float*)d_in[22];
-  const float* mapL_w = (const float*)d_in[23]; const float* mapL_b = (const float*)d_in[24];
-  const float* fin_w  = (const float*)d_in[25]; const float* fin_b  = (const float*)d_in[26];
-  float* out = (float*)d_out;
+  Args a;
+  a.z       = (const float*)d_in[0];
+  a.hs_grid = (const float*)d_in[1];
+  a.hs_key  = (const float*)d_in[2];
+  a.lig_rep = (const float*)d_in[3];
+  a.hs_rec  = (const float*)d_in[4];
+  a.wRl     = (const float*)d_in[5];
+  a.mask    = (const int*)d_in[6];
+  a.wsrc[0] = (const float*)d_in[7];   a.wra_b = (const float*)d_in[8];
+  a.wsrc[1] = (const float*)d_in[9];   a.wrh_b = (const float*)d_in[10];
+  a.wsrc[2] = (const float*)d_in[11];  a.wla_b = (const float*)d_in[12];
+  a.wsrc[3] = (const float*)d_in[13];  a.wlh_b = (const float*)d_in[14];
+  a.z1w     = (const float*)d_in[15];
+  a.wsrc[4] = (const float*)d_in[17];
+  a.wcR_w   = (const float*)d_in[17];
+  a.wsrc[5] = (const float*)d_in[19];  a.wcl_b = (const float*)d_in[20];
+  a.wsrc[6] = (const float*)d_in[21];  a.kR_b  = (const float*)d_in[22];
+  a.mapL_w  = (const float*)d_in[23];  a.mapL_b = (const float*)d_in[24];
+  a.fin_w   = (const float*)d_in[25];  a.fin_b  = (const float*)d_in[26];
+  a.out = (float*)d_out;
 
   float* w = (float*)d_ws;
-  float* wT    = w;
-  float* ra    = wT + 7 * 16384;
-  float* att   = ra + Bb * Gg * Mm;
-  float* laNum = att + Bb * Gg * Kk;
-  float* laDen = laNum + Bb * NCH * Kk * Mm;
-  float* la    = laDen + Bb * NCH * Kk * Mm;
-  float* attlP = la + Bb * Kk * Mm;
-  float* attrPM = attlP + Bb * 8 * 64;
-  float* attrPS = attrPM + Bb * 8 * 64;
-  float* att_r = attrPS + Bb * 8 * 64;
-  float* Lk    = att_r + Bb * Gg;
-  float* scores = Lk + Bb * Kk * Mm;
-
-  float* pmT  = laNum;
-  float* psT  = laNum + 32768;
-  float* uP   = laNum + 65536;
-  float* w1P  = laNum + 73728;
-  float* w2P  = laNum + 81920;
-  float* w0P  = laNum + 90112;
-  float* v1   = laNum + 90176;
-  float* v2   = laNum + 91200;
-  float* sAv  = laNum + 92224;
-
-  P7 ptrs;
-  ptrs.p[0] = wra_w; ptrs.p[1] = wrh_w; ptrs.p[2] = wla_w; ptrs.p[3] = wlh_w;
-  ptrs.p[4] = wcR_w; ptrs.p[5] = wcl_w; ptrs.p[6] = kR_w;
-
-  kA<<<Bb * NCH + 112, 1024, 0, stream>>>(z, hs_grid, hs_key, z1_w, ptrs, wT,
-                                          ra, att, laNum, laDen);
-  kB<<<448, 256, 0, stream>>>(laNum, laDen, la, att, attlP, attrPM, attrPS,
-                              hs_key, wT, wcR_w, wcl_b, Lk);
-  kC<<<576, 256, 0, stream>>>(att, attrPM, attrPS, att_r, hs_rec, Lk,
-                              w_mask, w_Rl, scores, pmT, psT);
-  kD<<<136, 512, 0, stream>>>(scores, hs_rec, pmT, psT, attlP, att_r,
-                              ra, hs_grid, la, hs_key,
-                              uP, w1P, w2P, w0P, v1, v2, sAv);
-  kE<<<Bb, 256, 0, stream>>>(uP, w1P, w2P, w0P, v1, v2, sAv, wT,
-                             wra_b, wrh_b, wla_b, wlh_b, kR_b, lig_rep,
-                             mapL_w, mapL_b, fin_w, fin_b, out);
+  a.wT    = w;
+  a.ra    = a.wT + 7 * 16384;
+  a.att   = a.ra + Bb * Gg * Mm;
+  a.laNum = a.att + Bb * Gg * Kk;
+  a.laDen = a.laNum + Bb * NCH * Kk * Mm;
+  a.la    = a.laDen + Bb * NCH * Kk * Mm;
+  a.attlP = a.la + Bb * Kk * Mm;
+  a.attrPM = a.attlP + Bb * 8 * 64;
+  a.attrPS = a.attrPM + Bb * 8 * 64;
+  a.att_r = a.attrPS + Bb * 8 * 64;
+  a.Lk    = a.att_r + Bb * Gg;
+  a.scores = a.Lk + Bb * Kk * Mm;
+
+  a.pmT = a.laNum;
+  a.psT = a.laNum + 32768;
+  a.uP  = a.laNum + 65536;
+  a.w1P = a.laNum + 73728;
+  a.w2P = a.laNum + 81920;
+  a.w0P = a.laNum + 90112;
+  a.v1  = a.laNum + 90176;
+  a.v2  = a.laNum + 91200;
+  a.sAv = a.laNum + 92224;
+
+  void* params[] = { (void*)&a };
+  hipLaunchCooperativeKernel((const void*)fused, dim3(256), dim3(1024),
+                             params, 0, stream);
 }
```

After: 238.1 us. +159.9%, slower.
